# Performance work log

Measured on AMD Instinct MI355X. Metric: run time of the kernel, lower is better.

Reference implementation:

```python
import jax, jax.numpy as jnp
import numpy as np

N_QUBITS = 8

# Quantum circuit math: starting from |0...0>, apply RX(x_i) then RY(theta_i) on each
# wire independently (product state preserved). Exact PauliZ expectation per wire:
#   RX(x)|0> = cos(x/2)|0> - i sin(x/2)|1>;  after RY(t):
#   <Z> = cos(x) * cos(t)
# This is the exact closed form of the full state-vector simulation the torch module runs.

def setup_inputs() -> dict:
    key = jax.random.key(0)
    k1, k2, k3, k4 = jax.random.split(key, 4)
    B, S, D, F = 4, 4096, 1024, 4096
    x = jax.random.normal(k1, (B, S, D), dtype=jnp.float32)
    theta = jax.random.normal(k2, (N_QUBITS,), dtype=jnp.float32)
    W1 = jax.random.normal(k3, (F, N_QUBITS), dtype=jnp.float32) * (1.0 / np.sqrt(N_QUBITS))
    W2 = jax.random.normal(k4, (D, F), dtype=jnp.float32) * (1.0 / np.sqrt(F))
    return {"x": x, "theta": theta, "W1": W1, "W2": W2}


def reference(x, theta, W1, W2):
    # Encoder only reads the first n_qubits features of each token.
    z = jnp.cos(x[..., :N_QUBITS]) * jnp.cos(theta)          # [B, S, Q] PauliZ expectations
    h = jax.nn.relu(jnp.einsum('bsq,fq->bsf', z, W1))        # [B, S, ffn_dim]
    return jnp.einsum('bsf,df->bsd', h, W2)                  # [B, S, embed_dim]
```

## Files before the change

kernel.cpp:

```cpp
#include <hip/hip_runtime.h>
#include <hip/hip_bf16.h>
#include <math.h>


using f32x4  = __attribute__((ext_vector_type(4))) float;
using bf16x8 = __attribute__((ext_vector_type(8))) short;
using i32x4  = __attribute__((ext_vector_type(4))) int;

#define M_TOT 16384
#define N_TOT 1024
#define K_TOT 4096
#define NKT   128
#define TILEB 16384

static const size_t H_BYTES   = (size_t)M_TOT * K_TOT * 2;
static const size_t W2B_BYTES = (size_t)N_TOT * K_TOT * 2;
static const size_t WS_NEED   = H_BYTES + W2B_BYTES;

#define SWZ32(row, bytecol) ((bytecol) ^ ((((row) >> 1) & 3) << 4))

#define GLD16(gp, lp) __builtin_amdgcn_global_load_lds( \
    (const __attribute__((address_space(1))) unsigned int*)(const void*)(gp), \
    (__attribute__((address_space(3))) unsigned int*)(void*)(lp), 16, 0, 0)

static __device__ inline unsigned short f2bf(float f) {
    __hip_bfloat16 b = __float2bfloat16(f);
    unsigned short u;
    __builtin_memcpy(&u, &b, 2);
    return u;
}

__global__ __launch_bounds__(256)
void k_prep(const float* __restrict__ x, const float* __restrict__ theta,
            const float* __restrict__ W1, const float* __restrict__ W2,
            char* __restrict__ hws, char* __restrict__ w2ws)
{
    __shared__ float sZ[256 * 8];
    __shared__ float sW[128 * 8];
    const int tid = threadIdx.x;

    if (blockIdx.x < 2048) {
        const int bx = blockIdx.x >> 5;
        const int by = blockIdx.x & 31;

        {
            const float* xp = x + ((size_t)bx * 256 + tid) * 1024;
            f32x4 a = *reinterpret_cast<const f32x4*>(xp);
            f32x4 b = *reinterpret_cast<const f32x4*>(xp + 4);
            #pragma unroll
            for (int q = 0; q < 4; ++q) {
                sZ[tid * 8 + q]     = cosf(a[q]) * cosf(theta[q]);
                sZ[tid * 8 + 4 + q] = cosf(b[q]) * cosf(theta[q + 4]);
            }
        }
        *reinterpret_cast<f32x4*>(&sW[tid * 4]) =
            *reinterpret_cast<const f32x4*>(W1 + (size_t)by * 1024 + tid * 4);
        __syncthreads();

        const int tm = tid >> 4;
        const int tk = tid & 15;

        f32x4 wA[8], wB[8];
        #pragma unroll
        for (int kk = 0; kk < 8; ++kk) {
            wA[kk] = *reinterpret_cast<const f32x4*>(&sW[(tk * 8 + kk) * 8]);
            wB[kk] = *reinterpret_cast<const f32x4*>(&sW[(tk * 8 + kk) * 8 + 4]);
        }

        const int kt    = by * 4 + (tk >> 2);
        const int slotb = (tk & 3) * 16;
        char* tb = hws + ((size_t)bx * NKT + kt) * TILEB;

        #pragma unroll
        for (int i = 0; i < 16; ++i) {
            const int row = tm * 16 + i;
            f32x4 za = *reinterpret_cast<const f32x4*>(&sZ[row * 8]);
            f32x4 zb = *reinterpret_cast<const f32x4*>(&sZ[row * 8 + 4]);
            unsigned hu[8];
            #pragma unroll
            for (int kk = 0; kk < 8; ++kk) {
                float h = 0.f;
                #pragma unroll
                for (int q = 0; q < 4; ++q) {
                    h = fmaf(za[q], wA[kk][q], h);
                    h = fmaf(zb[q], wB[kk][q], h);
                }
                hu[kk] = (unsigned)f2bf(fmaxf(h, 0.f));
            }
            i32x4 pk;
            pk[0] = (int)(hu[0] | (hu[1] << 16));
            pk[1] = (int)(hu[2] | (hu[3] << 16));
            pk[2] = (int)(hu[4] | (hu[5] << 16));
            pk[3] = (int)(hu[6] | (hu[7] << 16));
            *reinterpret_cast<i32x4*>(tb + row * 64 + SWZ32(row, slotb)) = pk;
        }
    } else {
        const int gt = (blockIdx.x - 2048) * 256 + tid;
        const int n  = gt >> 9;
        const int k8 = gt & 511;
        const float* p = W2 + (size_t)n * K_TOT + k8 * 8;
        f32x4 a = *reinterpret_cast<const f32x4*>(p);
        f32x4 b = *reinterpret_cast<const f32x4*>(p + 4);
        i32x4 pk;
        pk[0] = (int)((unsigned)f2bf(a[0]) | ((unsigned)f2bf(a[1]) << 16));
        pk[1] = (int)((unsigned)f2bf(a[2]) | ((unsigned)f2bf(a[3]) << 16));
        pk[2] = (int)((unsigned)f2bf(b[0]) | ((unsigned)f2bf(b[1]) << 16));
        pk[3] = (int)((unsigned)f2bf(b[2]) | ((unsigned)f2bf(b[3]) << 16));
        const int nt = n >> 8, row = n & 255, kt = k8 >> 2, slotb = (k8 & 3) * 16;
        char* dst = w2ws + ((size_t)nt * NKT + kt) * TILEB + row * 64 + slotb;
        *reinterpret_cast<i32x4*>(dst) = pk;
    }
}


#define DS_FRAGS(RD, BUF1) do {                                                   \
    const char* sa_ = ldsA + (BUF1) * 16384;                                      \
    _Pragma("unroll")                                                             \
    for (int i = 0; i < 8; ++i)                                                   \
        Pa[RD][i] = *reinterpret_cast<const bf16x8*>(sa_ + aoff + i * 1024);      \
} while (0)

#define B_LOAD(RD, KT1) do {                                                      \
    const char* gb_ = bT + (size_t)(KT1) * TILEB + bofsG;                         \
    _Pragma("unroll")                                                             \
    for (int j = 0; j < 4; ++j)                                                   \
        Pb[RD][j] = *reinterpret_cast<const bf16x8*>(gb_ + j * 1024);             \
} while (0)

#define STAGE2(KT3, BUF3) do {                                                    \
    const char* ga_ = aT + (size_t)(KT3) * TILEB;                                 \
    GLD16(ga_ + gofs,        ldsA + (BUF3) * 16384 + lofs);                       \
    GLD16(ga_ + 8192 + gofs, ldsA + (BUF3) * 16384 + 8192 + lofs);                \
} while (0)

#define MFMA32(USE) do {                                                          \
    __builtin_amdgcn_s_setprio(1);                                                \
    _Pragma("unroll")                                                             \
    for (int i = 0; i < 8; ++i)                                                   \
        _Pragma("unroll")                                                         \
        for (int j = 0; j < 4; ++j)                                               \
            acc[i][j] = __builtin_amdgcn_mfma_f32_16x16x32_bf16(Pa[USE][i], Pb[USE][j], acc[i][j], 0, 0, 0); \
    __builtin_amdgcn_s_setprio(0);                                                \
} while (0)

#define PHASE(BUF, KT, WN, DOB, DOSTAGE) do {                                     \
    asm volatile("s_waitcnt vmcnt(" #WN ")" ::: "memory");                        \
    __builtin_amdgcn_sched_barrier(0);                                            \
    __builtin_amdgcn_s_barrier();                                                 \
    __builtin_amdgcn_sched_barrier(0);                                            \
    DS_FRAGS(((BUF) + 1) & 1, ((BUF) + 1) & 3);                                   \
    if (DOB)     B_LOAD(((BUF) + 1) & 1, (KT) + 1);                               \
    if (DOSTAGE) STAGE2((KT) + 3, ((BUF) + 3) & 3);                               \
    __builtin_amdgcn_sched_barrier(0);                                            \
    MFMA32((BUF) & 1);                                                            \
} while (0)

__global__ __launch_bounds__(512, 2)
void k_gemm(const char* __restrict__ hws, const char* __restrict__ w2ws,
            float* __restrict__ out)
{
    __shared__ __align__(16) char ldsA[65536];

    const int tid  = threadIdx.x;
    const int lane = tid & 63;
    const int wave = tid >> 6;
    const int wm = wave >> 2;
    const int wn = wave & 3;
    const int mt = blockIdx.x;
    const int nt = blockIdx.y;

    const char* aT = hws  + (size_t)mt * NKT * TILEB;
    const char* bT = w2ws + (size_t)nt * NKT * TILEB;

    const int l16 = lane & 15;
    const int lkb = (lane >> 4) * 16;
    const int arow0 = wm * 128 + l16;
    const int aoff  = arow0 * 64 + SWZ32(arow0, lkb);
    const int bofsG = wn * 4096 + l16 * 64 + (lane >> 4) * 16;

    const int gofs = tid * 16;
    const int lofs = wave * 1024;

    bf16x8 Pa[2][8];
    bf16x8 Pb[2][4];

    f32x4 acc[8][4];
    #pragma unroll
    for (int i = 0; i < 8; ++i)
        #pragma unroll
        for (int j = 0; j < 4; ++j)
            acc[i][j] = {0.f, 0.f, 0.f, 0.f};

    STAGE2(0, 0);
    STAGE2(1, 1);
    STAGE2(2, 2);
    B_LOAD(0, 0);
    asm volatile("s_waitcnt vmcnt(8)" ::: "memory");
    __builtin_amdgcn_sched_barrier(0);
    __builtin_amdgcn_s_barrier();
    __builtin_amdgcn_sched_barrier(0);
    DS_FRAGS(0, 0);

    #pragma unroll 1
    for (int t = 0; t < 124; t += 4) {
        PHASE(0, t,     6, 1, 1);
        PHASE(1, t + 1, 6, 1, 1);
        PHASE(2, t + 2, 6, 1, 1);
        PHASE(3, t + 3, 6, 1, 1);
    }
    PHASE(0, 124, 6, 1, 1);
    PHASE(1, 125, 6, 1, 0);
    PHASE(2, 126, 4, 1, 0);
    __builtin_amdgcn_sched_barrier(0);
    MFMA32(1);

    const int orow0 = mt * 256 + wm * 128 + (lane >> 4) * 4;
    const int ocol0 = nt * 256 + wn * 64 + l16;
    #pragma unroll
    for (int i = 0; i < 8; ++i)
        #pragma unroll
        for (int j = 0; j < 4; ++j)
            #pragma unroll
            for (int jj = 0; jj < 4; ++jj)
                out[(size_t)(orow0 + i * 16 + jj) * N_TOT + (ocol0 + j * 16)] = acc[i][j][jj];
}

__global__ __launch_bounds__(256, 3)
void qffn_fused(const float* __restrict__ x, const float* __restrict__ theta,
                const float* __restrict__ W1, const float* __restrict__ W2,
                float* __restrict__ out)
{
    __shared__ __align__(16) unsigned short sA[128 * 64];
    __shared__ __align__(16) unsigned short sB[128 * 64];

    const int tid  = threadIdx.x;
    const int lane = tid & 63;
    const int wave = tid >> 6;
    const int m0 = blockIdx.x * 128;
    const int n0 = blockIdx.y * 128;

    const int arow = tid & 127;
    float zc[8];
    {
        const float* xp = x + (size_t)(m0 + arow) * 1024;
        f32x4 x0 = *reinterpret_cast<const f32x4*>(xp);
        f32x4 x1 = *reinterpret_cast<const f32x4*>(xp + 4);
        #pragma unroll
        for (int q = 0; q < 4; ++q) {
            zc[q]     = cosf(x0[q]) * cosf(theta[q]);
            zc[q + 4] = cosf(x1[q]) * cosf(theta[q + 4]);
        }
    }

    f32x4 acc[4][4];
    #pragma unroll
    for (int i = 0; i < 4; ++i)
        #pragma unroll
        for (int j = 0; j < 4; ++j)
            acc[i][j] = {0.f, 0.f, 0.f, 0.f};

    const int wr  = (wave >> 1) * 64;
    const int wc  = (wave & 1) * 64;
    const int l16 = lane & 15;
    const int lk8 = (lane >> 4) * 8;

    for (int k0 = 0; k0 < K_TOT; k0 += 64) {
        #pragma unroll
        for (int g = 0; g < 4; ++g) {
            const int cg  = (tid >> 7) + 2 * g;
            const int cgu = __builtin_amdgcn_readfirstlane(cg);
            const float* w1p = W1 + (size_t)(k0 + cgu * 8) * 8;
            i32x4 pk;
            #pragma unroll
            for (int p = 0; p < 4; ++p) {
                float h0 = 0.f, h1 = 0.f;
                #pragma unroll
                for (int q = 0; q < 8; ++q) {
                    h0 = fmaf(zc[q], w1p[(2 * p) * 8 + q], h0);
                    h1 = fmaf(zc[q], w1p[(2 * p + 1) * 8 + q], h1);
                }
                pk[p] = (int)(((unsigned)f2bf(fmaxf(h0, 0.f))) |
                              (((unsigned)f2bf(fmaxf(h1, 0.f))) << 16));
            }
            const int off = (arow * 64 + cg * 8) ^ ((arow & 7) << 3);
            *reinterpret_cast<i32x4*>(&sA[off]) = pk;
        }
        {
            const int fi = tid & 15;
            const int rb = tid >> 4;
            #pragma unroll
            for (int r = 0; r < 8; ++r) {
                const int row = rb + r * 16;
                f32x4 v = *(reinterpret_cast<const f32x4*>(W2 + (size_t)(n0 + row) * K_TOT + k0) + fi);
                unsigned p0 = (unsigned)f2bf(v[0]) | ((unsigned)f2bf(v[1]) << 16);
                unsigned p1 = (unsigned)f2bf(v[2]) | ((unsigned)f2bf(v[3]) << 16);
                const int off = (row * 64 + fi * 4) ^ ((row & 7) << 3);
                *reinterpret_cast<unsigned*>(&sB[off])     = p0;
                *reinterpret_cast<unsigned*>(&sB[off + 2]) = p1;
            }
        }
        __syncthreads();

        #pragma unroll
        for (int s = 0; s < 2; ++s) {
            bf16x8 af[4], bfr[4];
            #pragma unroll
            for (int i = 0; i < 4; ++i) {
                const int row = wr + i * 16 + l16;
                const int off = (row * 64 + s * 32 + lk8) ^ ((row & 7) << 3);
                af[i] = *reinterpret_cast<const bf16x8*>(&sA[off]);
            }
            #pragma unroll
            for (int j = 0; j < 4; ++j) {
                const int row = wc + j * 16 + l16;
                const int off = (row * 64 + s * 32 + lk8) ^ ((row & 7) << 3);
                bfr[j] = *reinterpret_cast<const bf16x8*>(&sB[off]);
            }
            #pragma unroll
            for (int i = 0; i < 4; ++i)
                #pragma unroll
                for (int j = 0; j < 4; ++j)
                    acc[i][j] = __builtin_amdgcn_mfma_f32_16x16x32_bf16(af[i], bfr[j], acc[i][j], 0, 0, 0);
        }
        __syncthreads();
    }

    const int orow0 = m0 + wr + (lane >> 4) * 4;
    const int ocol0 = n0 + wc + l16;
    #pragma unroll
    for (int i = 0; i < 4; ++i)
        #pragma unroll
        for (int j = 0; j < 4; ++j)
            #pragma unroll
            for (int jj = 0; jj < 4; ++jj)
                out[(size_t)(orow0 + i * 16 + jj) * N_TOT + (ocol0 + j * 16)] = acc[i][j][jj];
}

extern "C" void kernel_launch(void* const* d_in, const int* in_sizes, int n_in,
                              void* d_out, int out_size, void* d_ws, size_t ws_size,
                              hipStream_t stream) {
    const float* x     = (const float*)d_in[0];
    const float* theta = (const float*)d_in[1];
    const float* W1    = (const float*)d_in[2];
    const float* W2    = (const float*)d_in[3];
    float* out = (float*)d_out;

    if (ws_size >= WS_NEED) {
        char* hws  = (char*)d_ws;
        char* w2ws = (char*)d_ws + H_BYTES;

        k_prep<<<dim3(4096), dim3(256), 0, stream>>>(x, theta, W1, W2, hws, w2ws);
        k_gemm<<<dim3(M_TOT / 256, N_TOT / 256), dim3(512), 0, stream>>>(hws, w2ws, out);
    } else {
        qffn_fused<<<dim3(M_TOT / 128, N_TOT / 128), dim3(256), 0, stream>>>(x, theta, W1, W2, out);
    }
}
```

Before: 162.8 us.

## Restructure GEMM to 256x128 tiles with triple-buffered LDS staging of A and B

```diff
diff --git a/kernel.cpp b/kernel.cpp
--- a/kernel.cpp
+++ b/kernel.cpp
@@ -11,13 +11,12 @@
 #define N_TOT 1024
 #define K_TOT 4096
 #define NKT   128
-#define TILEB 16384
+#define ATB   16384
+#define BTB   8192
 
 static const size_t H_BYTES   = (size_t)M_TOT * K_TOT * 2;
 static const size_t W2B_BYTES = (size_t)N_TOT * K_TOT * 2;
 static const size_t WS_NEED   = H_BYTES + W2B_BYTES;
-
-#define SWZ32(row, bytecol) ((bytecol) ^ ((((row) >> 1) & 3) << 4))
 
 #define GLD16(gp, lp) __builtin_amdgcn_global_load_lds( \
     (const __attribute__((address_space(1))) unsigned int*)(const void*)(gp), \
@@ -29,6 +28,8 @@
     __builtin_memcpy(&u, &b, 2);
     return u;
 }
+
+#define PR_OFF(r, s) (((r) >> 1) * 128 + (((r) & 1) << 6) + (s) * 16)
 
 __global__ __launch_bounds__(256)
 void k_prep(const float* __restrict__ x, const float* __restrict__ theta,
@@ -67,15 +68,15 @@
             wB[kk] = *reinterpret_cast<const f32x4*>(&sW[(tk * 8 + kk) * 8 + 4]);
         }
 
-        const int kt    = by * 4 + (tk >> 2);
-        const int slotb = (tk & 3) * 16;
-        char* tb = hws + ((size_t)bx * NKT + kt) * TILEB;
+        const int kt = by * 4 + (tk >> 2);
+        const int s  = tk & 3;
+        char* tb = hws + ((size_t)(bx * NKT + kt)) * ATB;
 
         #pragma unroll
         for (int i = 0; i < 16; ++i) {
-            const int row = tm * 16 + i;
-            f32x4 za = *reinterpret_cast<const f32x4*>(&sZ[row * 8]);
-            f32x4 zb = *reinterpret_cast<const f32x4*>(&sZ[row * 8 + 4]);
+            const int R = tm * 16 + i;
+            f32x4 za = *reinterpret_cast<const f32x4*>(&sZ[R * 8]);
+            f32x4 zb = *reinterpret_cast<const f32x4*>(&sZ[R * 8 + 4]);
             unsigned hu[8];
             #pragma unroll
             for (int kk = 0; kk < 8; ++kk) {
@@ -92,7 +93,7 @@
             pk[1] = (int)(hu[2] | (hu[3] << 16));
             pk[2] = (int)(hu[4] | (hu[5] << 16));
             pk[3] = (int)(hu[6] | (hu[7] << 16));
-            *reinterpret_cast<i32x4*>(tb + row * 64 + SWZ32(row, slotb)) = pk;
+            *reinterpret_cast<i32x4*>(tb + PR_OFF(R, s)) = pk;
         }
     } else {
         const int gt = (blockIdx.x - 2048) * 256 + tid;
@@ -106,83 +107,101 @@
         pk[1] = (int)((unsigned)f2bf(a[2]) | ((unsigned)f2bf(a[3]) << 16));
         pk[2] = (int)((unsigned)f2bf(b[0]) | ((unsigned)f2bf(b[1]) << 16));
         pk[3] = (int)((unsigned)f2bf(b[2]) | ((unsigned)f2bf(b[3]) << 16));
-        const int nt = n >> 8, row = n & 255, kt = k8 >> 2, slotb = (k8 & 3) * 16;
-        char* dst = w2ws + ((size_t)nt * NKT + kt) * TILEB + row * 64 + slotb;
+        const int nt = n >> 7, r = n & 127, kt = k8 >> 2, s = k8 & 3;
+        char* dst = w2ws + ((size_t)(nt * NKT + kt)) * BTB + PR_OFF(r, s);
         *reinterpret_cast<i32x4*>(dst) = pk;
     }
 }
 
 
-#define DS_FRAGS(RD, BUF1) do {                                                   \
-    const char* sa_ = ldsA + (BUF1) * 16384;                                      \
-    _Pragma("unroll")                                                             \
-    for (int i = 0; i < 8; ++i)                                                   \
-        Pa[RD][i] = *reinterpret_cast<const bf16x8*>(sa_ + aoff + i * 1024);      \
+#define STAGE_T(T, RB2) do {                                              \
+    const char* ga_ = aT + (size_t)(T) * ATB;                             \
+    const char* gb_ = bT + (size_t)(T) * BTB;                             \
+    char* la_ = lds + (RB2) * 24576;                                      \
+    GLD16(ga_ + tid * 16,         la_ + tid * 16);                        \
+    GLD16(ga_ + 4096 + tid * 16,  la_ + 4096 + tid * 16);                 \
+    GLD16(ga_ + 8192 + tid * 16,  la_ + 8192 + tid * 16);                 \
+    GLD16(ga_ + 12288 + tid * 16, la_ + 12288 + tid * 16);                \
+    GLD16(gb_ + tid * 16,         la_ + 16384 + tid * 16);                \
+    GLD16(gb_ + 4096 + tid * 16,  la_ + 16384 + 4096 + tid * 16);         \
 } while (0)
 
-#define B_LOAD(RD, KT1) do {                                                      \
-    const char* gb_ = bT + (size_t)(KT1) * TILEB + bofsG;                         \
-    _Pragma("unroll")                                                             \
-    for (int j = 0; j < 4; ++j)                                                   \
-        Pb[RD][j] = *reinterpret_cast<const bf16x8*>(gb_ + j * 1024);             \
+#define TILE(RB, T, DOSTAGE, WN) do {                                     \
+    const char* sa_ = lds + (RB) * 24576;                                 \
+    const char* sb_ = sa_ + 16384;                                        \
+    bf16x8 af[8], bfr[4];                                                 \
+    _Pragma("unroll")                                                     \
+    for (int i = 0; i < 8; ++i)                                           \
+        af[i] = *reinterpret_cast<const bf16x8*>(sa_ + aoff[i]);          \
+    _Pragma("unroll")                                                     \
+    for (int j = 0; j < 4; ++j)                                           \
+        bfr[j] = *reinterpret_cast<const bf16x8*>(sb_ + boff[j]);         \
+    if (DOSTAGE) STAGE_T((T) + 2, ((RB) + 2) % 3);                        \
+    asm volatile("s_waitcnt lgkmcnt(0)" ::: "memory");                    \
+    __builtin_amdgcn_sched_barrier(0);                                    \
+    __builtin_amdgcn_s_setprio(1);                                        \
+    _Pragma("unroll")                                                     \
+    for (int i = 0; i < 8; ++i)                                           \
+        _Pragma("unroll")                                                 \
+        for (int j = 0; j < 4; ++j)                                       \
+            acc[i][j] = __builtin_amdgcn_mfma_f32_16x16x32_bf16(af[i], bfr[j], acc[i][j], 0, 0, 0); \
+    __builtin_amdgcn_s_setprio(0);                                        \
+    asm volatile("s_waitcnt vmcnt(" #WN ")" ::: "memory");                \
+    __builtin_amdgcn_sched_barrier(0);                                    \
+    __builtin_amdgcn_s_barrier();                                         \
+    __builtin_amdgcn_sched_barrier(0);                                    \
 } while (0)
 
-#define STAGE2(KT3, BUF3) do {                                                    \
-    const char* ga_ = aT + (size_t)(KT3) * TILEB;                                 \
-    GLD16(ga_ + gofs,        ldsA + (BUF3) * 16384 + lofs);                       \
-    GLD16(ga_ + 8192 + gofs, ldsA + (BUF3) * 16384 + 8192 + lofs);                \
+#define TILE_LAST(RB) do {                                                \
+    const char* sa_ = lds + (RB) * 24576;                                 \
+    const char* sb_ = sa_ + 16384;                                        \
+    bf16x8 af[8], bfr[4];                                                 \
+    _Pragma("unroll")                                                     \
+    for (int i = 0; i < 8; ++i)                                           \
+        af[i] = *reinterpret_cast<const bf16x8*>(sa_ + aoff[i]);          \
+    _Pragma("unroll")                                                     \
+    for (int j = 0; j < 4; ++j)                                           \
+        bfr[j] = *reinterpret_cast<const bf16x8*>(sb_ + boff[j]);         \
+    asm volatile("s_waitcnt lgkmcnt(0)" ::: "memory");                    \
+    __builtin_amdgcn_sched_barrier(0);                                    \
+    _Pragma("unroll")                                                     \
+    for (int i = 0; i < 8; ++i)                                           \
+        _Pragma("unroll")                                                 \
+        for (int j = 0; j < 4; ++j)                                       \
+            acc[i][j] = __builtin_amdgcn_mfma_f32_16x16x32_bf16(af[i], bfr[j], acc[i][j], 0, 0, 0); \
 } while (0)
 
-#define MFMA32(USE) do {                                                          \
-    __builtin_amdgcn_s_setprio(1);                                                \
-    _Pragma("unroll")                                                             \
-    for (int i = 0; i < 8; ++i)                                                   \
-        _Pragma("unroll")                                                         \
-        for (int j = 0; j < 4; ++j)                                               \
-            acc[i][j] = __builtin_amdgcn_mfma_f32_16x16x32_bf16(Pa[USE][i], Pb[USE][j], acc[i][j], 0, 0, 0); \
-    __builtin_amdgcn_s_setprio(0);                                                \
-} while (0)
-
-#define PHASE(BUF, KT, WN, DOB, DOSTAGE) do {                                     \
-    asm volatile("s_waitcnt vmcnt(" #WN ")" ::: "memory");                        \
-    __builtin_amdgcn_sched_barrier(0);                                            \
-    __builtin_amdgcn_s_barrier();                                                 \
-    __builtin_amdgcn_sched_barrier(0);                                            \
-    DS_FRAGS(((BUF) + 1) & 1, ((BUF) + 1) & 3);                                   \
-    if (DOB)     B_LOAD(((BUF) + 1) & 1, (KT) + 1);                               \
-    if (DOSTAGE) STAGE2((KT) + 3, ((BUF) + 3) & 3);                               \
-    __builtin_amdgcn_sched_barrier(0);                                            \
-    MFMA32((BUF) & 1);                                                            \
-} while (0)
-
-__global__ __launch_bounds__(512, 2)
+__global__ __launch_bounds__(256, 2)
 void k_gemm(const char* __restrict__ hws, const char* __restrict__ w2ws,
             float* __restrict__ out)
 {
-    __shared__ __align__(16) char ldsA[65536];
+    __shared__ __align__(16) char lds[73728];
 
     const int tid  = threadIdx.x;
     const int lane = tid & 63;
     const int wave = tid >> 6;
-    const int wm = wave >> 2;
-    const int wn = wave & 3;
-    const int mt = blockIdx.x;
-    const int nt = blockIdx.y;
-
-    const char* aT = hws  + (size_t)mt * NKT * TILEB;
-    const char* bT = w2ws + (size_t)nt * NKT * TILEB;
+    const int wm = wave >> 1;
+    const int wn = wave & 1;
+    const int bid = blockIdx.x;
+    const int ntb = bid & 7;
+    const int mt  = bid >> 3;
+
+    const char* aT = hws  + (size_t)mt  * NKT * ATB;
+    const char* bT = w2ws + (size_t)ntb * NKT * BTB;
 
     const int l16 = lane & 15;
-    const int lkb = (lane >> 4) * 16;
-    const int arow0 = wm * 128 + l16;
-    const int aoff  = arow0 * 64 + SWZ32(arow0, lkb);
-    const int bofsG = wn * 4096 + l16 * 64 + (lane >> 4) * 16;
-
-    const int gofs = tid * 16;
-    const int lofs = wave * 1024;
-
-    bf16x8 Pa[2][8];
-    bf16x8 Pb[2][4];
+    const int sl  = lane >> 4;
+    int aoff[8], boff[4];
+    #pragma unroll
+    for (int i = 0; i < 8; ++i) {
+        const int r = wm * 128 + i * 16 + l16;
+        aoff[i] = PR_OFF(r, sl);
+    }
+    #pragma unroll
+    for (int j = 0; j < 4; ++j) {
+        const int r = wn * 64 + j * 16 + l16;
+        boff[j] = PR_OFF(r, sl);
+    }
 
     f32x4 acc[8][4];
     #pragma unroll
@@ -191,31 +210,24 @@
         for (int j = 0; j < 4; ++j)
             acc[i][j] = {0.f, 0.f, 0.f, 0.f};
 
-    STAGE2(0, 0);
-    STAGE2(1, 1);
-    STAGE2(2, 2);
-    B_LOAD(0, 0);
-    asm volatile("s_waitcnt vmcnt(8)" ::: "memory");
+    STAGE_T(0, 0);
+    STAGE_T(1, 1);
+    asm volatile("s_waitcnt vmcnt(6)" ::: "memory");
     __builtin_amdgcn_sched_barrier(0);
     __builtin_amdgcn_s_barrier();
     __builtin_amdgcn_sched_barrier(0);
-    DS_FRAGS(0, 0);
 
     #pragma unroll 1
-    for (int t = 0; t < 124; t += 4) {
-        PHASE(0, t,     6, 1, 1);
-        PHASE(1, t + 1, 6, 1, 1);
-        PHASE(2, t + 2, 6, 1, 1);
-        PHASE(3, t + 3, 6, 1, 1);
-    }
-    PHASE(0, 124, 6, 1, 1);
-    PHASE(1, 125, 6, 1, 0);
-    PHASE(2, 126, 4, 1, 0);
-    __builtin_amdgcn_sched_barrier(0);
-    MFMA32(1);
+    for (int t = 0; t < 126; t += 3) {
+        TILE(0, t,     1, 6);
+        TILE(1, t + 1, 1, 6);
+        TILE(2, t + 2, 1, 6);
+    }
+    TILE(0, 126, 0, 0);
+    TILE_LAST(1);
 
     const int orow0 = mt * 256 + wm * 128 + (lane >> 4) * 4;
-    const int ocol0 = nt * 256 + wn * 64 + l16;
+    const int ocol0 = ntb * 128 + wn * 64 + l16;
     #pragma unroll
     for (int i = 0; i < 8; ++i)
         #pragma unroll
@@ -350,7 +362,7 @@
         char* w2ws = (char*)d_ws + H_BYTES;
 
         k_prep<<<dim3(4096), dim3(256), 0, stream>>>(x, theta, W1, W2, hws, w2ws);
-        k_gemm<<<dim3(M_TOT / 256, N_TOT / 256), dim3(512), 0, stream>>>(hws, w2ws, out);
+        k_gemm<<<dim3(512), dim3(256), 0, stream>>>(hws, w2ws, out);
     } else {
         qffn_fused<<<dim3(M_TOT / 128, N_TOT / 128), dim3(256), 0, stream>>>(x, theta, W1, W2, out);
     }
```

New measurement: 201.2 us. 1.24x slower.
